# Kernel optimization log

Measured on AMD Instinct MI355X. Metric: run time of the kernel, lower is better.

Reference implementation:

```python
import jax, jax.numpy as jnp
import numpy as np

N_NODES = 50000
N_EDGES = 1600000
C_IN = 19
C_OUT = 128


def _branch(x, W, b, aW, ab, edge_index):
    # x: [N, C_in]; edge_index: [2, E] with row0=src(j), row1=dst(i) (PyG source_to_target)
    xt = x @ W.T + b                       # [N, C_out]
    src, dst = edge_index[0], edge_index[1]
    x_j = xt[src]                          # [E, C_out]
    x_i = xt[dst]                          # [E, C_out]
    # attn_lin on concat([x_i, x_j]) == x_i @ aW[:, :C].T + x_j @ aW[:, C:].T + ab
    logits = x_i @ aW[:, :C_OUT].T + x_j @ aW[:, C_OUT:].T + ab  # [E, 1]
    attn = jax.nn.sigmoid(logits)
    msg = attn * x_j                       # [E, C_out]
    return jax.ops.segment_sum(msg, dst, num_segments=N_NODES)  # [N, C_out]


def setup_inputs() -> dict:
    key = jax.random.key(0)
    ks = jax.random.split(key, 12)
    s_in = 1.0 / np.sqrt(C_IN)
    s_attn = 1.0 / np.sqrt(2 * C_OUT)
    return {
        "x": jax.random.normal(ks[0], (N_NODES, C_IN), jnp.float32),
        "hyperedge_index": jax.random.randint(ks[1], (2, N_EDGES), 0, N_NODES, jnp.int32),
        "knn_edge_index": jax.random.randint(ks[2], (2, N_EDGES), 0, N_NODES, jnp.int32),
        "hyper_lin_W": jax.random.uniform(ks[3], (C_OUT, C_IN), jnp.float32, -s_in, s_in),
        "hyper_lin_b": jax.random.uniform(ks[4], (C_OUT,), jnp.float32, -s_in, s_in),
        "hyper_attn_W": jax.random.uniform(ks[5], (1, 2 * C_OUT), jnp.float32, -s_attn, s_attn),
        "hyper_attn_b": jax.random.uniform(ks[6], (1,), jnp.float32, -s_attn, s_attn),
        "knn_lin_W": jax.random.uniform(ks[7], (C_OUT, C_IN), jnp.float32, -s_in, s_in),
        "knn_lin_b": jax.random.uniform(ks[8], (C_OUT,), jnp.float32, -s_in, s_in),
        "knn_attn_W": jax.random.uniform(ks[9], (1, 2 * C_OUT), jnp.float32, -s_attn, s_attn),
        "knn_attn_b": jax.random.uniform(ks[10], (1,), jnp.float32, -s_attn, s_attn),
        "gate_W": jax.random.uniform(ks[11], (2, 2 * C_OUT), jnp.float32, -s_attn, s_attn),
        "gate_b": jnp.zeros((2,), jnp.float32),
    }


def reference(x, hyperedge_index, knn_edge_index, hyper_lin_W, hyper_lin_b,
              hyper_attn_W, hyper_attn_b, knn_lin_W, knn_lin_b, knn_attn_W,
              knn_attn_b, gate_W, gate_b):
    hyper_out = _branch(x, hyper_lin_W, hyper_lin_b, hyper_attn_W, hyper_attn_b, hyperedge_index)
    knn_out = _branch(x, knn_lin_W, knn_lin_b, knn_attn_W, knn_attn_b, knn_edge_index)
    # gate_lin on concat([hyper_out, knn_out])
    gate_logits = hyper_out @ gate_W[:, :C_OUT].T + knn_out @ gate_W[:, C_OUT:].T + gate_b  # [N, 2]
    gate = jax.nn.sigmoid(gate_logits)
    return gate[:, 0:1] * hyper_out + gate[:, 1:2] * knn_out
```

## Files before the change

kernel.cpp:

```cpp
#include <hip/hip_runtime.h>
#include <hip/hip_bf16.h>

#define N_NODES 50000
#define N_EDGES 1600000
#define C_IN 19
#define C_OUT 128
#define NPB 40
#define TBLOCKS (N_NODES / NPB)
#define CAP 92
#define NBUCK 391
#define BNODE 128
#define EPB 2560
#define PBLK (N_EDGES / EPB)
#define P3T 320
#define NCOL (2 * NBUCK)
#define COLCAP 4608
#define SCT 640

typedef unsigned short ushort_t;
typedef unsigned int uint_t;

__device__ __forceinline__ float sigmoidf(float v) { return 1.0f / (1.0f + expf(-v)); }


__global__ __launch_bounds__(128) void node_p1(
    const float* __restrict__ x,
    const float* __restrict__ Wh, const float* __restrict__ bh,
    const float* __restrict__ aWh, const float* __restrict__ abh,
    const float* __restrict__ Wk, const float* __restrict__ bk,
    const float* __restrict__ aWk, const float* __restrict__ abk,
    __hip_bfloat16* __restrict__ xt_h, __hip_bfloat16* __restrict__ xt_k,
    float* __restrict__ sh_i, float* __restrict__ sh_j,
    float* __restrict__ sk_i, float* __restrict__ sk_j,
    const int* __restrict__ hdst, const int* __restrict__ kdst,
    int* __restrict__ counts)
{
    __shared__ float sW[2 * C_OUT * C_IN];
    __shared__ float xrow[NPB * C_IN];
    __shared__ float su[80];
    __shared__ int hist[NBUCK];

    const int c = threadIdx.x;

    if (blockIdx.x >= TBLOCKS) {
        const int blk0 = blockIdx.x - TBLOCKS;
        const int g = blk0 >= PBLK;
        const int blk = blk0 - g * PBLK;
        const int* dst = g ? kdst : hdst;
        for (int i = c; i < NBUCK; i += 128) hist[i] = 0;
        __syncthreads();
        const int4* dst4 = reinterpret_cast<const int4*>(dst + blk * EPB);
#pragma unroll
        for (int i = 0; i < 5; ++i) {
            const int4 v = dst4[c + i * 128];
            atomicAdd(&hist[v.x >> 7], 1);
            atomicAdd(&hist[v.y >> 7], 1);
            atomicAdd(&hist[v.z >> 7], 1);
            atomicAdd(&hist[v.w >> 7], 1);
        }
        __syncthreads();
        for (int i = c; i < NBUCK; i += 128)
            counts[(g * NBUCK + i) * PBLK + blk] = hist[i];
        return;
    }

    const float4* Wh4 = reinterpret_cast<const float4*>(Wh);
    const float4* Wk4 = reinterpret_cast<const float4*>(Wk);
    float4* sW4 = reinterpret_cast<float4*>(sW);
    for (int i = c; i < 608; i += 128) { sW4[i] = Wh4[i]; sW4[608 + i] = Wk4[i]; }

    const int base_n = blockIdx.x * NPB;
    const float4* x4 = reinterpret_cast<const float4*>(x + (size_t)base_n * C_IN);
    float4* xr4 = reinterpret_cast<float4*>(xrow);
    for (int i = c; i < NPB * C_IN / 4; i += 128) xr4[i] = x4[i];
    __syncthreads();

    float wh[C_IN], wk[C_IN];
#pragma unroll
    for (int k = 0; k < C_IN; ++k) {
        wh[k] = sW[c * C_IN + k];
        wk[k] = sW[2432 + c * C_IN + k];
    }
    const float bhc = bh[c], bkc = bk[c];

    for (int i = 0; i < NPB; ++i) {
        float ah = bhc, ak = bkc;
#pragma unroll
        for (int k = 0; k < C_IN; ++k) {
            const float xv = xrow[i * C_IN + k];
            ah = fmaf(xv, wh[k], ah);
            ak = fmaf(xv, wk[k], ak);
        }
        const int n = base_n + i;
        xt_h[(size_t)n * C_OUT + c] = __float2bfloat16(ah);
        xt_k[(size_t)n * C_OUT + c] = __float2bfloat16(ak);
    }

    if (c < 76) {
        const int v = c / 19, k = c % 19;
        const float* aW = (v < 2) ? aWh : aWk;
        const float* Wbase = sW + ((v < 2) ? 0 : 2432);
        const int half = (v & 1) * C_OUT;
        float s = 0.f;
        for (int cc = 0; cc < C_OUT; ++cc)
            s = fmaf(aW[half + cc], Wbase[cc * C_IN + k], s);
        su[c] = s;
    } else if (c < 80) {
        const int v = c - 76;
        const float* aW = (v < 2) ? aWh : aWk;
        const float* b = (v < 2) ? bh : bk;
        const int half = (v & 1) * C_OUT;
        float s = 0.f;
        for (int cc = 0; cc < C_OUT; ++cc)
            s = fmaf(aW[half + cc], b[cc], s);
        if ((v & 1) == 0) s += (v < 2) ? abh[0] : abk[0];
        su[c] = s;
    }
    __syncthreads();

    for (int i = c; i < NPB; i += 128) {
        const int n = base_n + i;
        float s0 = su[76], s1 = su[77], s2 = su[78], s3 = su[79];
#pragma unroll
        for (int k = 0; k < C_IN; ++k) {
            const float xv = xrow[i * C_IN + k];
            s0 = fmaf(xv, su[k], s0);
            s1 = fmaf(xv, su[19 + k], s1);
            s2 = fmaf(xv, su[38 + k], s2);
            s3 = fmaf(xv, su[57 + k], s3);
        }
        sh_i[n] = s0; sh_j[n] = s1; sk_i[n] = s2; sk_j[n] = s3;
    }
}

__global__ __launch_bounds__(SCT) void p2a(int* __restrict__ counts, int* __restrict__ coltot)
{
    const int col = blockIdx.x;
    const int t = threadIdx.x;
    const int lane = t & 63, w = t >> 6;
    __shared__ int wtot[SCT / 64];

    const int v = (t < PBLK) ? counts[col * PBLK + t] : 0;
    int inc = v;
    for (int o = 1; o < 64; o <<= 1) {
        const int u = __shfl_up(inc, o);
        if (lane >= o) inc += u;
    }
    if (lane == 63) wtot[w] = inc;
    __syncthreads();
    if (t < SCT / 64) {
        int s = wtot[t];
        int run = s;
        for (int o = 1; o < SCT / 64; o <<= 1) {
            const int u = __shfl_up(run, o, 16);
            if (t >= o) run += u;
        }
        wtot[t] = run - s;
    }
    __syncthreads();
    const int ex = inc - v + wtot[w];
    if (t < PBLK) counts[col * PBLK + t] = ex;
    if (t == PBLK - 1) coltot[col] = ex + v;
}

__global__ __launch_bounds__(P3T) void p3_part(
    const int* __restrict__ hei, const int* __restrict__ kei,
    const float* __restrict__ sh_i, const float* __restrict__ sh_j,
    const float* __restrict__ sk_i, const float* __restrict__ sk_j,
    const int* __restrict__ counts,
    uint_t* __restrict__ part32)
{
    const int g = blockIdx.x >= PBLK;
    const int blk = blockIdx.x - g * PBLK;
    const int* ei = g ? kei : hei;
    const float* s_i = g ? sk_i : sh_i;
    const float* s_j = g ? sk_j : sh_j;

    __shared__ int cur[NBUCK];
    __shared__ int gbase[NBUCK];
    const int t = threadIdx.x;
    for (int i = t; i < NBUCK; i += P3T) {
        cur[i] = 0;
        gbase[i] = counts[(g * NBUCK + i) * PBLK + blk];
    }
    __syncthreads();

    const int base = blk * EPB;
    const int4* src4 = reinterpret_cast<const int4*>(ei + base);
    const int4* dst4 = reinterpret_cast<const int4*>(ei + N_EDGES + base);
    const int4 sa = src4[t], sb = src4[t + P3T];
    const int4 da = dst4[t], db = dst4[t + P3T];

    int s[8] = {sa.x, sa.y, sa.z, sa.w, sb.x, sb.y, sb.z, sb.w};
    int d[8] = {da.x, da.y, da.z, da.w, db.x, db.y, db.z, db.w};
    float si[8], sj[8];
#pragma unroll
    for (int i = 0; i < 8; ++i) { si[i] = s_i[d[i]]; sj[i] = s_j[s[i]]; }
    uint_t w9[8];
#pragma unroll
    for (int i = 0; i < 8; ++i)
        w9[i] = (uint_t)(sigmoidf(si[i] + sj[i]) * 511.f + 0.5f);
#pragma unroll
    for (int i = 0; i < 8; ++i) {
        const int b = d[i] >> 7;
        const int r = atomicAdd(&cur[b], 1);
        const int off = gbase[b] + r;
        if (off < COLCAP) {
            const size_t col = (size_t)(g * NBUCK + b);
            part32[col * COLCAP + off] =
                ((uint_t)s[i] << 16) | ((uint_t)(d[i] & 127) << 9) | w9[i];
        }
    }
}

__global__ __launch_bounds__(256) void p4_final(
    const uint_t* __restrict__ part32,
    const int* __restrict__ coltot,
    uint_t* __restrict__ finrec, int* __restrict__ cnt)
{
    const int col = blockIdx.x;
    const int g = col >= NBUCK;
    const int b = col - g * NBUCK;
    __shared__ int cur[BNODE];
    const int t = threadIdx.x;
    if (t < BNODE) cur[t] = 0;
    __syncthreads();
    const int start = col * COLCAP;
    int len = coltot[col];
    len = len < COLCAP ? len : COLCAP;
    const size_t fbase = (size_t)(g * N_NODES + (b << 7)) * CAP;

    int i = t;
    for (; i + 768 < len; i += 1024) {
        const uint_t v0 = part32[start + i];
        const uint_t v1 = part32[start + i + 256];
        const uint_t v2 = part32[start + i + 512];
        const uint_t v3 = part32[start + i + 768];
        const int d0 = (v0 >> 9) & 127, d1 = (v1 >> 9) & 127;
        const int d2 = (v2 >> 9) & 127, d3 = (v3 >> 9) & 127;
        const int r0 = atomicAdd(&cur[d0], 1);
        const int r1 = atomicAdd(&cur[d1], 1);
        const int r2 = atomicAdd(&cur[d2], 1);
        const int r3 = atomicAdd(&cur[d3], 1);
        if (r0 < CAP) finrec[fbase + (size_t)d0 * CAP + r0] = v0;
        if (r1 < CAP) finrec[fbase + (size_t)d1 * CAP + r1] = v1;
        if (r2 < CAP) finrec[fbase + (size_t)d2 * CAP + r2] = v2;
        if (r3 < CAP) finrec[fbase + (size_t)d3 * CAP + r3] = v3;
    }
    for (; i < len; i += 256) {
        const uint_t v = part32[start + i];
        const int dl = (v >> 9) & 127;
        const int r = atomicAdd(&cur[dl], 1);
        if (r < CAP) finrec[fbase + (size_t)dl * CAP + r] = v;
    }
    __syncthreads();
    if (t < BNODE) {
        const int node = (b << 7) + t;
        if (node < N_NODES) {
            const int c = cur[t];
            cnt[g * N_NODES + node] = c < CAP ? c : CAP;
        }
    }
}

struct Acc8 { float a0, a1, a2, a3, a4, a5, a6, a7; };

__device__ __forceinline__ void qfma(Acc8& a, const uint4 u, const float wgt)
{
    a.a0 = fmaf(wgt, __uint_as_float(u.x << 16), a.a0);
    a.a1 = fmaf(wgt, __uint_as_float(u.x & 0xffff0000u), a.a1);
    a.a2 = fmaf(wgt, __uint_as_float(u.y << 16), a.a2);
    a.a3 = fmaf(wgt, __uint_as_float(u.y & 0xffff0000u), a.a3);
    a.a4 = fmaf(wgt, __uint_as_float(u.z << 16), a.a4);
    a.a5 = fmaf(wgt, __uint_as_float(u.z & 0xffff0000u), a.a5);
    a.a6 = fmaf(wgt, __uint_as_float(u.w << 16), a.a6);
    a.a7 = fmaf(wgt, __uint_as_float(u.w & 0xffff0000u), a.a7);
}

__global__ __launch_bounds__(128) void gather_gate(
    const __hip_bfloat16* __restrict__ xt_h, const __hip_bfloat16* __restrict__ xt_k,
    const uint_t* __restrict__ finrec, const int* __restrict__ cnt,
    const float* __restrict__ gW, const float* __restrict__ gb,
    float* __restrict__ out)
{
    const int n = blockIdx.x;
    const int tid = threadIdx.x, lane = tid & 63, wid = tid >> 6;
    const int li = lane & 15, q = lane >> 4;

    const ushort_t* xt = reinterpret_cast<const ushort_t*>(wid ? xt_k : xt_h);
    const uint_t* rec = finrec + (size_t)(wid * N_NODES + n) * CAP;
    const int end = cnt[wid * N_NODES + n];

    Acc8 acc = {0.f, 0.f, 0.f, 0.f, 0.f, 0.f, 0.f, 0.f};
    const uint_t choff = (uint_t)(li << 3);
    const float wscale = 1.0f / 511.f;

    int p = 0;
    for (; p + 16 <= end; p += 16) {
        const uint_t rv0 = rec[p + q];
        const uint_t rv1 = rec[p + 4 + q];
        const uint_t rv2 = rec[p + 8 + q];
        const uint_t rv3 = rec[p + 12 + q];
        const uint4 u0 = *reinterpret_cast<const uint4*>(xt + (((size_t)(rv0 >> 16)) << 7) + choff);
        const uint4 u1 = *reinterpret_cast<const uint4*>(xt + (((size_t)(rv1 >> 16)) << 7) + choff);
        const uint4 u2 = *reinterpret_cast<const uint4*>(xt + (((size_t)(rv2 >> 16)) << 7) + choff);
        const uint4 u3 = *reinterpret_cast<const uint4*>(xt + (((size_t)(rv3 >> 16)) << 7) + choff);
        const float w0 = (float)(rv0 & 0x1ffu) * wscale;
        const float w1 = (float)(rv1 & 0x1ffu) * wscale;
        const float w2 = (float)(rv2 & 0x1ffu) * wscale;
        const float w3 = (float)(rv3 & 0x1ffu) * wscale;
        qfma(acc, u0, w0); qfma(acc, u1, w1); qfma(acc, u2, w2); qfma(acc, u3, w3);
    }
    for (; p < end; p += 4) {
        const int e = p + q;
        const uint_t rv = rec[e < end ? e : end - 1];
        const float wgt = (e < end) ? (float)(rv & 0x1ffu) * wscale : 0.f;
        const uint4 u = *reinterpret_cast<const uint4*>(xt + (((size_t)(rv >> 16)) << 7) + choff);
        qfma(acc, u, wgt);
    }

    __shared__ float sacc[2][4][C_OUT + 8];
    *reinterpret_cast<float4*>(&sacc[wid][q][li << 3]) = make_float4(acc.a0, acc.a1, acc.a2, acc.a3);
    *reinterpret_cast<float4*>(&sacc[wid][q][(li << 3) + 4]) = make_float4(acc.a4, acc.a5, acc.a6, acc.a7);
    __syncthreads();

    const float h = sacc[0][0][tid] + sacc[0][1][tid] + sacc[0][2][tid] + sacc[0][3][tid];
    const float k = sacc[1][0][tid] + sacc[1][1][tid] + sacc[1][2][tid] + sacc[1][3][tid];

    float2 part = make_float2(fmaf(h, gW[tid], k * gW[C_OUT + tid]),
                              fmaf(h, gW[2 * C_OUT + tid], k * gW[3 * C_OUT + tid]));
    for (int o = 32; o > 0; o >>= 1) {
        part.x += __shfl_xor(part.x, o);
        part.y += __shfl_xor(part.y, o);
    }
    __shared__ float2 wsum[2];
    __shared__ float gg[2];
    if (lane == 0) wsum[wid] = part;
    __syncthreads();
    if (tid == 0) {
        gg[0] = sigmoidf(wsum[0].x + wsum[1].x + gb[0]);
        gg[1] = sigmoidf(wsum[0].y + wsum[1].y + gb[1]);
    }
    __syncthreads();
    out[(size_t)n * C_OUT + tid] = gg[0] * h + gg[1] * k;
}

extern "C" void kernel_launch(void* const* d_in, const int* in_sizes, int n_in,
                              void* d_out, int out_size, void* d_ws, size_t ws_size,
                              hipStream_t stream) {
    const float* x   = (const float*)d_in[0];
    const int*   hei = (const int*)d_in[1];
    const int*   kei = (const int*)d_in[2];
    const float* hW  = (const float*)d_in[3];
    const float* hb  = (const float*)d_in[4];
    const float* haW = (const float*)d_in[5];
    const float* hab = (const float*)d_in[6];
    const float* kW  = (const float*)d_in[7];
    const float* kb  = (const float*)d_in[8];
    const float* kaW = (const float*)d_in[9];
    const float* kab = (const float*)d_in[10];
    const float* gW  = (const float*)d_in[11];
    const float* gb  = (const float*)d_in[12];
    float* out = (float*)d_out;

    const size_t NC = (size_t)N_NODES * C_OUT;
    char* base = (char*)d_ws;

    __hip_bfloat16* xt_h = (__hip_bfloat16*)base;
    __hip_bfloat16* xt_k = xt_h + NC;
    float* sh_i = (float*)(xt_k + NC);
    float* sh_j = sh_i + N_NODES;
    float* sk_i = sh_j + N_NODES;
    float* sk_j = sk_i + N_NODES;
    int* counts   = (int*)(sk_j + N_NODES);
    int* coltot   = counts + NCOL * PBLK;
    int* cnt      = coltot + NCOL;
    uint_t* part32 = (uint_t*)(cnt + 2 * N_NODES);
    uint_t* finrec = part32 + (size_t)NCOL * COLCAP;

    node_p1<<<TBLOCKS + 2 * PBLK, 128, 0, stream>>>(
        x, hW, hb, haW, hab, kW, kb, kaW, kab,
        xt_h, xt_k, sh_i, sh_j, sk_i, sk_j,
        hei + N_EDGES, kei + N_EDGES, counts);

    p2a<<<NCOL, SCT, 0, stream>>>(counts, coltot);

    p3_part<<<2 * PBLK, P3T, 0, stream>>>(
        hei, kei, sh_i, sh_j, sk_i, sk_j,
        counts, part32);

    p4_final<<<NCOL, 256, 0, stream>>>(
        part32, coltot, finrec, cnt);

    gather_gate<<<N_NODES, 128, 0, stream>>>(
        xt_h, xt_k, finrec, cnt, gW, gb, out);
}
```

Before: 193.7 us.

## Quantize transformed node features to int8 with per-node scales for gather

Node features after the linear layer are now stored as unsigned 8-bit values with a per-row absmax scale and a zero point of 128, replacing bf16. The gather kernel loads 8 bytes per lane instead of 16 and folds the per-source scale into the edge weight. It then subtracts the zero-point offset using the summed weights. This halves the bytes of the random gather traffic, but adds per-node reductions and barriers in the producer kernel plus an extra scale load per edge. It also lowers accuracy, which may exceed tolerance.

```diff
diff --git a/kernel.cpp b/kernel.cpp
--- a/kernel.cpp
+++ b/kernel.cpp
@@ -19,6 +19,7 @@
 
 typedef unsigned short ushort_t;
 typedef unsigned int uint_t;
+typedef unsigned char uchar_t;
 
 __device__ __forceinline__ float sigmoidf(float v) { return 1.0f / (1.0f + expf(-v)); }
 
@@ -29,7 +30,8 @@
     const float* __restrict__ aWh, const float* __restrict__ abh,
     const float* __restrict__ Wk, const float* __restrict__ bk,
     const float* __restrict__ aWk, const float* __restrict__ abk,
-    __hip_bfloat16* __restrict__ xt_h, __hip_bfloat16* __restrict__ xt_k,
+    uchar_t* __restrict__ xt8_h, uchar_t* __restrict__ xt8_k,
+    float* __restrict__ scales,
     float* __restrict__ sh_i, float* __restrict__ sh_j,
     float* __restrict__ sk_i, float* __restrict__ sk_j,
     const int* __restrict__ hdst, const int* __restrict__ kdst,
@@ -38,6 +40,8 @@
     __shared__ float sW[2 * C_OUT * C_IN];
     __shared__ float xrow[NPB * C_IN];
     __shared__ float su[80];
+    __shared__ uint_t qb[2 * NPB * 32];
+    __shared__ float sred[2][4];
     __shared__ int hist[NBUCK];
 
     const int c = threadIdx.x;
@@ -64,6 +68,8 @@
         return;
     }
 
+    const int lane = c & 63, wid2 = c >> 6;
+
     const float4* Wh4 = reinterpret_cast<const float4*>(Wh);
     const float4* Wk4 = reinterpret_cast<const float4*>(Wk);
     float4* sW4 = reinterpret_cast<float4*>(sW);
@@ -91,9 +97,27 @@
             ah = fmaf(xv, wh[k], ah);
             ak = fmaf(xv, wk[k], ak);
         }
+        float mh = fabsf(ah), mk = fabsf(ak);
+        for (int o = 32; o > 0; o >>= 1) {
+            mh = fmaxf(mh, __shfl_xor(mh, o));
+            mk = fmaxf(mk, __shfl_xor(mk, o));
+        }
+        const int slot = i & 1;
+        if (lane == 0) { sred[slot][wid2 * 2] = mh; sred[slot][wid2 * 2 + 1] = mk; }
+        __syncthreads();
+        mh = fmaxf(sred[slot][0], sred[slot][2]);
+        mk = fmaxf(sred[slot][1], sred[slot][3]);
+        const float sch = fmaxf(mh, 1e-20f) * (1.0f / 127.0f);
+        const float sck = fmaxf(mk, 1e-20f) * (1.0f / 127.0f);
+        int qh = (int)rintf(ah / sch) + 128;
+        int qk = (int)rintf(ak / sck) + 128;
+        qh = qh < 0 ? 0 : (qh > 255 ? 255 : qh);
+        qk = qk < 0 ? 0 : (qk > 255 ? 255 : qk);
+        reinterpret_cast<uchar_t*>(qb)[(size_t)i * 128 + c] = (uchar_t)qh;
+        reinterpret_cast<uchar_t*>(qb)[(size_t)(NPB + i) * 128 + c] = (uchar_t)qk;
         const int n = base_n + i;
-        xt_h[(size_t)n * C_OUT + c] = __float2bfloat16(ah);
-        xt_k[(size_t)n * C_OUT + c] = __float2bfloat16(ak);
+        if (c == 0) scales[n] = sch;
+        if (c == 1) scales[N_NODES + n] = sck;
     }
 
     if (c < 76) {
@@ -131,6 +155,13 @@
         }
         sh_i[n] = s0; sh_j[n] = s1; sk_i[n] = s2; sk_j[n] = s3;
     }
+
+    uint_t* xh32 = reinterpret_cast<uint_t*>(xt8_h + (size_t)base_n * 128);
+    uint_t* xk32 = reinterpret_cast<uint_t*>(xt8_k + (size_t)base_n * 128);
+    for (int j = c; j < NPB * 32; j += 128) {
+        xh32[j] = qb[j];
+        xk32[j] = qb[NPB * 32 + j];
+    }
 }
 
 __global__ __launch_bounds__(SCT) void p2a(int* __restrict__ counts, int* __restrict__ coltot)
@@ -265,20 +296,21 @@
 
 struct Acc8 { float a0, a1, a2, a3, a4, a5, a6, a7; };
 
-__device__ __forceinline__ void qfma(Acc8& a, const uint4 u, const float wgt)
-{
-    a.a0 = fmaf(wgt, __uint_as_float(u.x << 16), a.a0);
-    a.a1 = fmaf(wgt, __uint_as_float(u.x & 0xffff0000u), a.a1);
-    a.a2 = fmaf(wgt, __uint_as_float(u.y << 16), a.a2);
-    a.a3 = fmaf(wgt, __uint_as_float(u.y & 0xffff0000u), a.a3);
-    a.a4 = fmaf(wgt, __uint_as_float(u.z << 16), a.a4);
-    a.a5 = fmaf(wgt, __uint_as_float(u.z & 0xffff0000u), a.a5);
-    a.a6 = fmaf(wgt, __uint_as_float(u.w << 16), a.a6);
-    a.a7 = fmaf(wgt, __uint_as_float(u.w & 0xffff0000u), a.a7);
+__device__ __forceinline__ void qfma8(Acc8& a, const uint2 u, const float w)
+{
+    a.a0 = fmaf(w, (float)(u.x & 0xffu), a.a0);
+    a.a1 = fmaf(w, (float)((u.x >> 8) & 0xffu), a.a1);
+    a.a2 = fmaf(w, (float)((u.x >> 16) & 0xffu), a.a2);
+    a.a3 = fmaf(w, (float)(u.x >> 24), a.a3);
+    a.a4 = fmaf(w, (float)(u.y & 0xffu), a.a4);
+    a.a5 = fmaf(w, (float)((u.y >> 8) & 0xffu), a.a5);
+    a.a6 = fmaf(w, (float)((u.y >> 16) & 0xffu), a.a6);
+    a.a7 = fmaf(w, (float)(u.y >> 24), a.a7);
 }
 
 __global__ __launch_bounds__(128) void gather_gate(
-    const __hip_bfloat16* __restrict__ xt_h, const __hip_bfloat16* __restrict__ xt_k,
+    const uchar_t* __restrict__ xt8_h, const uchar_t* __restrict__ xt8_k,
+    const float* __restrict__ scales,
     const uint_t* __restrict__ finrec, const int* __restrict__ cnt,
     const float* __restrict__ gW, const float* __restrict__ gb,
     float* __restrict__ out)
@@ -287,11 +319,13 @@
     const int tid = threadIdx.x, lane = tid & 63, wid = tid >> 6;
     const int li = lane & 15, q = lane >> 4;
 
-    const ushort_t* xt = reinterpret_cast<const ushort_t*>(wid ? xt_k : xt_h);
+    const uchar_t* xt = wid ? xt8_k : xt8_h;
+    const float* scl = scales + (size_t)wid * N_NODES;
     const uint_t* rec = finrec + (size_t)(wid * N_NODES + n) * CAP;
     const int end = cnt[wid * N_NODES + n];
 
     Acc8 acc = {0.f, 0.f, 0.f, 0.f, 0.f, 0.f, 0.f, 0.f};
+    float csum = 0.f;
     const uint_t choff = (uint_t)(li << 3);
     const float wscale = 1.0f / 511.f;
 
@@ -301,23 +335,30 @@
         const uint_t rv1 = rec[p + 4 + q];
         const uint_t rv2 = rec[p + 8 + q];
         const uint_t rv3 = rec[p + 12 + q];
-        const uint4 u0 = *reinterpret_cast<const uint4*>(xt + (((size_t)(rv0 >> 16)) << 7) + choff);
-        const uint4 u1 = *reinterpret_cast<const uint4*>(xt + (((size_t)(rv1 >> 16)) << 7) + choff);
-        const uint4 u2 = *reinterpret_cast<const uint4*>(xt + (((size_t)(rv2 >> 16)) << 7) + choff);
-        const uint4 u3 = *reinterpret_cast<const uint4*>(xt + (((size_t)(rv3 >> 16)) << 7) + choff);
-        const float w0 = (float)(rv0 & 0x1ffu) * wscale;
-        const float w1 = (float)(rv1 & 0x1ffu) * wscale;
-        const float w2 = (float)(rv2 & 0x1ffu) * wscale;
-        const float w3 = (float)(rv3 & 0x1ffu) * wscale;
-        qfma(acc, u0, w0); qfma(acc, u1, w1); qfma(acc, u2, w2); qfma(acc, u3, w3);
+        const int s0 = rv0 >> 16, s1 = rv1 >> 16, s2 = rv2 >> 16, s3 = rv3 >> 16;
+        const uint2 u0 = *reinterpret_cast<const uint2*>(xt + (((size_t)s0) << 7) + choff);
+        const uint2 u1 = *reinterpret_cast<const uint2*>(xt + (((size_t)s1) << 7) + choff);
+        const uint2 u2 = *reinterpret_cast<const uint2*>(xt + (((size_t)s2) << 7) + choff);
+        const uint2 u3 = *reinterpret_cast<const uint2*>(xt + (((size_t)s3) << 7) + choff);
+        const float a0 = (float)(rv0 & 0x1ffu) * wscale * scl[s0];
+        const float a1 = (float)(rv1 & 0x1ffu) * wscale * scl[s1];
+        const float a2 = (float)(rv2 & 0x1ffu) * wscale * scl[s2];
+        const float a3 = (float)(rv3 & 0x1ffu) * wscale * scl[s3];
+        qfma8(acc, u0, a0); qfma8(acc, u1, a1); qfma8(acc, u2, a2); qfma8(acc, u3, a3);
+        csum += a0 + a1 + a2 + a3;
     }
     for (; p < end; p += 4) {
         const int e = p + q;
         const uint_t rv = rec[e < end ? e : end - 1];
-        const float wgt = (e < end) ? (float)(rv & 0x1ffu) * wscale : 0.f;
-        const uint4 u = *reinterpret_cast<const uint4*>(xt + (((size_t)(rv >> 16)) << 7) + choff);
-        qfma(acc, u, wgt);
-    }
+        const int s = rv >> 16;
+        const float a = (e < end) ? (float)(rv & 0x1ffu) * wscale * scl[s] : 0.f;
+        const uint2 u = *reinterpret_cast<const uint2*>(xt + (((size_t)s) << 7) + choff);
+        qfma8(acc, u, a);
+        csum += a;
+    }
+    const float corr = 128.f * csum;
+    acc.a0 -= corr; acc.a1 -= corr; acc.a2 -= corr; acc.a3 -= corr;
+    acc.a4 -= corr; acc.a5 -= corr; acc.a6 -= corr; acc.a7 -= corr;
 
     __shared__ float sacc[2][4][C_OUT + 8];
     *reinterpret_cast<float4*>(&sacc[wid][q][li << 3]) = make_float4(acc.a0, acc.a1, acc.a2, acc.a3);
@@ -366,9 +407,10 @@
     const size_t NC = (size_t)N_NODES * C_OUT;
     char* base = (char*)d_ws;
 
-    __hip_bfloat16* xt_h = (__hip_bfloat16*)base;
-    __hip_bfloat16* xt_k = xt_h + NC;
-    float* sh_i = (float*)(xt_k + NC);
+    uchar_t* xt8_h = (uchar_t*)base;
+    uchar_t* xt8_k = xt8_h + NC;
+    float* scales = (float*)(xt8_k + NC);
+    float* sh_i = scales + 2 * N_NODES;
     float* sh_j = sh_i + N_NODES;
     float* sk_i = sh_j + N_NODES;
     float* sk_j = sk_i + N_NODES;
@@ -380,7 +422,7 @@
 
     node_p1<<<TBLOCKS + 2 * PBLK, 128, 0, stream>>>(
         x, hW, hb, haW, hab, kW, kb, kaW, kab,
-        xt_h, xt_k, sh_i, sh_j, sk_i, sk_j,
+        xt8_h, xt8_k, scales, sh_i, sh_j, sk_i, sk_j,
         hei + N_EDGES, kei + N_EDGES, counts);
 
     p2a<<<NCOL, SCT, 0, stream>>>(counts, coltot);
@@ -393,5 +435,5 @@
         part32, coltot, finrec, cnt);
 
     gather_gate<<<N_NODES, 128, 0, stream>>>(
-        xt_h, xt_k, finrec, cnt, gW, gb, out);
-}
+        xt8_h, xt8_k, scales, finrec, cnt, gW, gb, out);
+}
```

Result: slower. 221.1 us (+14.2%).
